# Performance work log

Hardware: AMD Instinct MI355X
Metric: run time of the kernel (lower is better)

Reference implementation:

```python
import jax, jax.numpy as jnp
import numpy as np

EMBED = 128
HEADS = 16
N = 10000
E = 160000
NEG_SLOPE = 0.2


def setup_inputs() -> dict:
    key = jax.random.key(0)
    ks = jax.random.split(key, 12)
    s = 0.05
    return {
        "x": jax.random.normal(ks[0], (N, EMBED), jnp.float32),
        "edge_index": jax.random.randint(ks[1], (2, E), 0, N, jnp.int64),
        # gat1: in=EMBED, out=EMBED, heads=16, concat
        "W1": jax.random.normal(ks[2], (EMBED, HEADS * EMBED), jnp.float32) * s,
        "a_src1": jax.random.normal(ks[3], (HEADS, EMBED), jnp.float32) * s,
        "a_dst1": jax.random.normal(ks[4], (HEADS, EMBED), jnp.float32) * s,
        "b1": jnp.zeros((HEADS * EMBED,), jnp.float32),
        # gat2: in=HEADS*EMBED, out=EMBED, heads=1, no concat
        "W2": jax.random.normal(ks[5], (HEADS * EMBED, EMBED), jnp.float32) * s,
        "a_src2": jax.random.normal(ks[6], (1, EMBED), jnp.float32) * s,
        "a_dst2": jax.random.normal(ks[7], (1, EMBED), jnp.float32) * s,
        "b2": jnp.zeros((EMBED,), jnp.float32),
        # classifier
        "Wc": jax.random.normal(ks[8], (EMBED, 1), jnp.float32) * s,
        "bc": jnp.zeros((1,), jnp.float32),
    }


def _gat_layer(x, src, dst, W, a_src, a_dst, b, heads, out_ch, n_nodes):
    # node projection: [N, H, C]
    h = (x @ W).reshape(n_nodes, heads, out_ch)
    # per-node attention logits [N, H]
    al_s = jnp.einsum('nhc,hc->nh', h, a_src)
    al_d = jnp.einsum('nhc,hc->nh', h, a_dst)
    # per-edge logits [E, H]
    e = jax.nn.leaky_relu(al_s[src] + al_d[dst], NEG_SLOPE)
    # segment softmax over incoming edges of each dst node
    m = jax.ops.segment_max(e, dst, num_segments=n_nodes)
    ex = jnp.exp(e - m[dst])
    z = jax.ops.segment_sum(ex, dst, num_segments=n_nodes)
    alpha = ex / (z[dst] + 1e-16)
    # weighted scatter-aggregate [N, H, C]
    msg = h[src] * alpha[:, :, None]
    out = jax.ops.segment_sum(msg, dst, num_segments=n_nodes)
    return out.reshape(n_nodes, heads * out_ch) + b


def reference(x, edge_index, W1, a_src1, a_dst1, b1, W2, a_src2, a_dst2, b2, Wc, bc):
    n_nodes = x.shape[0]
    # PyG GATConv default: add self loops
    loop = jnp.arange(n_nodes, dtype=edge_index.dtype)
    src = jnp.concatenate([edge_index[0], loop])
    dst = jnp.concatenate([edge_index[1], loop])
    h = _gat_layer(x, src, dst, W1, a_src1, a_dst1, b1, HEADS, EMBED, n_nodes)
    h = jax.nn.elu(h)
    h = _gat_layer(h, src, dst, W2, a_src2, a_dst2, b2, 1, EMBED, n_nodes)
    return h @ Wc + bc  # [N, 1]
```

## Files before the change

kernel.cpp:

```cpp
#include <hip/hip_runtime.h>
#include <hip/hip_bf16.h>

#define EMBED 128
#define HEADS 16
#define NEG 0.2f

typedef __attribute__((ext_vector_type(8))) short short8;
typedef __attribute__((ext_vector_type(4))) float floatx4;
typedef __attribute__((ext_vector_type(2))) float floatx2;

#define GLOAD_LDS16(g, l)                                                                  \
  __builtin_amdgcn_global_load_lds((const __attribute__((address_space(1))) unsigned int*)(g), \
                                   (__attribute__((address_space(3))) unsigned int*)(l),       \
                                   16, 0, 0)

static __device__ __forceinline__ float leaky(float x) { return x > 0.f ? x : NEG * x; }

static __device__ __forceinline__ short f2bf_bits(float f) {
  __hip_bfloat16 h = __float2bfloat16(f);
  union { __hip_bfloat16 b; short s; } u;
  u.b = h;
  return u.s;
}


__global__ __launch_bounds__(256) void k_prep_hist(const float* __restrict__ W1,
                                                   const float* __restrict__ a_src1,
                                                   const float* __restrict__ a_dst1,
                                                   const float* __restrict__ W2,
                                                   const float* __restrict__ a_src2,
                                                   const float* __restrict__ a_dst2,
                                                   const float* __restrict__ Wc,
                                                   const float* __restrict__ b2,
                                                   const float* __restrict__ bc,
                                                   float* __restrict__ wsAll,
                                                   float* __restrict__ uvec,
                                                   float* __restrict__ cconst,
                                                   short* __restrict__ hi,
                                                   short* __restrict__ lo,
                                                   const int* __restrict__ ei, int E, int N,
                                                   int* __restrict__ deg) {
  __shared__ float tile[64][65];
  int bx = blockIdx.x;
  if (bx < 64) {
    int h = bx & 15;
    int c0 = ((bx >> 4) & 1) * 64;
    int j0 = ((bx >> 5) & 1) * 64;
    int t = threadIdx.x;
#pragma unroll
    for (int i = 0; i < 4; ++i) {
      int idx4 = i * 256 + t;
      int c = idx4 >> 4, j4 = idx4 & 15;
      float4 v = *(const float4*)&W1[(size_t)(c0 + c) * 2048 + h * 128 + j0 + j4 * 4];
      tile[c][j4 * 4 + 0] = v.x;
      tile[c][j4 * 4 + 1] = v.y;
      tile[c][j4 * 4 + 2] = v.z;
      tile[c][j4 * 4 + 3] = v.w;
    }
    __syncthreads();
#pragma unroll
    for (int i = 0; i < 4; ++i) {
      int idx = i * 256 + t;
      int j = idx >> 4, c4 = idx & 15;
      unsigned short vh[4], vl[4];
#pragma unroll
      for (int ii = 0; ii < 4; ++ii) {
        float wv = tile[c4 * 4 + ii][j];
        short hb = f2bf_bits(wv);
        float hf = __uint_as_float(((unsigned int)(unsigned short)hb) << 16);
        vh[ii] = (unsigned short)hb;
        vl[ii] = (unsigned short)f2bf_bits(wv - hf);
      }
      size_t o = (size_t)h * 16384 + (size_t)(j0 + j) * 128 + c0 + c4 * 4;
      *(ushort4*)&hi[o] = make_ushort4(vh[0], vh[1], vh[2], vh[3]);
      *(ushort4*)&lo[o] = make_ushort4(vl[0], vl[1], vl[2], vl[3]);
    }
    return;
  }
  if (bx < 105) {
    int gid = (bx - 64) * 256 + threadIdx.x;
    if (gid < 4096) {
      int sel = gid >> 11;
      int id = gid & 2047;
      int h = id >> 7, k = id & 127;
      const float* av = sel ? a_dst1 : a_src1;
      float sum = 0.f;
      const float* wrow = W1 + (size_t)k * 2048 + h * 128;
      const float* arow = av + h * 128;
#pragma unroll 4
      for (int c = 0; c < 128; ++c) sum += wrow[c] * arow[c];
      wsAll[gid] = sum;
    } else if (gid < 10240) {
      int g = gid - 4096;
      int sel = g >> 11;
      int k = g & 2047;
      const float* v = sel == 0 ? Wc : (sel == 1 ? a_src2 : a_dst2);
      const float* wrow = W2 + (size_t)k * 128;
      float s = 0.f;
#pragma unroll 4
      for (int j = 0; j < 128; ++j) s += wrow[j] * v[j];
      uvec[g] = s;
    } else if (gid == 10240) {
      float s = 0.f;
      for (int j = 0; j < 128; ++j) s += b2[j] * Wc[j];
      *cconst = s + bc[0];
    }
    return;
  }
  int i = (bx - 105) * 256 + threadIdx.x;
  int Et = E + N;
  if (i >= Et) return;
  int d = (i < E) ? ei[E + i] : (i - E);
  atomicAdd(&deg[d], 1);
}


__global__ __launch_bounds__(256) void k_scan_al1(const int* __restrict__ deg,
                                                  int* __restrict__ row_ptr,
                                                  int* __restrict__ cursor,
                                                  const float* __restrict__ x,
                                                  const float* __restrict__ wsAll,
                                                  float* __restrict__ als,
                                                  float* __restrict__ ald, int N) {
  __shared__ float wss[128][16], wsd[128][16];
  __shared__ int wsum[4];
  int tid = threadIdx.x;
  int bx = blockIdx.x;

  if (bx == 0) {
    int lane = tid & 63, w = tid >> 6;
    int base = 0;
    for (int c0 = 0; c0 < N; c0 += 1024) {
      int i4 = c0 + tid * 4;
      int a0 = 0, a1 = 0, a2 = 0, a3 = 0;
      if (i4 + 3 < N) {
        int4 v = *(const int4*)&deg[i4];
        a0 = v.x; a1 = v.y; a2 = v.z; a3 = v.w;
      } else {
        if (i4 < N) a0 = deg[i4];
        if (i4 + 1 < N) a1 = deg[i4 + 1];
        if (i4 + 2 < N) a2 = deg[i4 + 2];
        if (i4 + 3 < N) a3 = deg[i4 + 3];
      }
      int tot = a0 + a1 + a2 + a3;
      int s = tot;
#pragma unroll
      for (int dd = 1; dd < 64; dd <<= 1) {
        int t = __shfl_up(s, dd);
        if (lane >= dd) s += t;
      }
      int wexcl = s - tot;
      if (lane == 63) wsum[w] = s;
      __syncthreads();
      int carry = 0, ctot = 0;
#pragma unroll
      for (int k = 0; k < 4; ++k) {
        int t = wsum[k];
        ctot += t;
        if (k < w) carry += t;
      }
      int p0 = base + carry + wexcl;
      int p1 = p0 + a0, p2 = p1 + a1, p3 = p2 + a2;
      if (i4 + 3 < N) {
        *(int4*)&row_ptr[i4] = make_int4(p0, p1, p2, p3);
        *(int4*)&cursor[i4] = make_int4(p0, p1, p2, p3);
      } else {
        if (i4 < N) { row_ptr[i4] = p0; cursor[i4] = p0; }
        if (i4 + 1 < N) { row_ptr[i4 + 1] = p1; cursor[i4 + 1] = p1; }
        if (i4 + 2 < N) { row_ptr[i4 + 2] = p2; cursor[i4 + 2] = p2; }
        if (i4 + 3 < N) { row_ptr[i4 + 3] = p3; cursor[i4 + 3] = p3; }
      }
      base += ctot;
      __syncthreads();
    }
    if (tid == 0) row_ptr[N] = base;
    return;
  }

  for (int i = tid; i < 2048; i += 256) {
    int h = i >> 7, c = i & 127;
    wss[c][h] = wsAll[i];
    wsd[c][h] = wsAll[2048 + i];
  }
  __syncthreads();
  int gid = (bx - 1) * 256 + tid;
  int n = gid >> 4, h = gid & 15;
  if (n >= N) return;
  const float4* xp = (const float4*)(x + (size_t)n * 128);
  float ps = 0.f, pd = 0.f;
#pragma unroll 8
  for (int c4 = 0; c4 < 32; ++c4) {
    float4 xv = xp[c4];
    int c = c4 * 4;
    ps += xv.x * wss[c][h] + xv.y * wss[c + 1][h] + xv.z * wss[c + 2][h] + xv.w * wss[c + 3][h];
    pd += xv.x * wsd[c][h] + xv.y * wsd[c + 1][h] + xv.z * wsd[c + 2][h] + xv.w * wsd[c + 3][h];
  }
  als[gid] = ps;
  ald[gid] = pd;
}


__global__ void k_scatter(const int* __restrict__ ei, int E, int N,
                          int* __restrict__ cursor, int* __restrict__ csr_src) {
  int i = blockIdx.x * blockDim.x + threadIdx.x;
  int Et = E + N;
  if (i >= Et) return;
  int s = (i < E) ? ei[i] : (i - E);
  int d = (i < E) ? ei[E + i] : (i - E);
  int pos = atomicAdd(&cursor[d], 1);
  csr_src[pos] = s;
}


__global__ __launch_bounds__(256) void k_attn1h(const float* __restrict__ x,
                                                const float* __restrict__ als,
                                                const float* __restrict__ ald,
                                                const int* __restrict__ row_ptr,
                                                const int* __restrict__ csr,
                                                __hip_bfloat16* __restrict__ xaggb,
                                                int N) {
  __shared__ float accsh[2][64][37];

  int tid = threadIdx.x;
  int w = tid >> 6, lane = tid & 63;
  int slot = w >> 1, half = w & 1;
  int d = blockIdx.x * 2 + slot;
  bool active = d < N;

  int e0 = 0, deg = 0;
  if (active) {
    e0 = row_ptr[d];
    deg = row_ptr[d + 1] - e0;
  }

  int g = lane >> 4, c8 = lane & 15;
  float4 aldh4 = make_float4(0.f, 0.f, 0.f, 0.f);
  if (active) aldh4 = *(const float4*)&ald[(size_t)d * 16 + g * 4];

  floatx2 acc2[4][4];
  float zacc[4] = {0.f, 0.f, 0.f, 0.f};
#pragma unroll
  for (int hh = 0; hh < 4; ++hh)
#pragma unroll
    for (int i = 0; i < 4; ++i) acc2[hh][i] = (floatx2){0.f, 0.f};

  if (active) {
    int sreg = 0;
    if (lane < deg) sreg = csr[e0 + lane];
    const float* xc = x + c8 * 8;

    int e = half;
    bool have = e < deg;
    float4 alC = make_float4(0.f, 0.f, 0.f, 0.f);
    float4 xaC = alC, xbC = alC;
    if (have) {
      int sC = (e < 64) ? __shfl(sreg, e) : csr[e0 + e];
      alC = *(const float4*)&als[(size_t)sC * 16 + g * 4];
      const float4* xp = (const float4*)(xc + (size_t)sC * 128);
      xaC = xp[0];
      xbC = xp[1];
    }
    while (have) {
      int e2 = e + 2;
      bool have2 = e2 < deg;
      float4 alN = alC, xaN = xaC, xbN = xbC;
      if (have2) {
        int sN = (e2 < 64) ? __shfl(sreg, e2) : csr[e0 + e2];
        alN = *(const float4*)&als[(size_t)sN * 16 + g * 4];
        const float4* xp2 = (const float4*)(xc + (size_t)sN * 128);
        xaN = xp2[0];
        xbN = xp2[1];
      }
      float ev0 = __expf(leaky(alC.x + aldh4.x));
      float ev1 = __expf(leaky(alC.y + aldh4.y));
      float ev2 = __expf(leaky(alC.z + aldh4.z));
      float ev3 = __expf(leaky(alC.w + aldh4.w));
      zacc[0] += ev0; zacc[1] += ev1; zacc[2] += ev2; zacc[3] += ev3;
      floatx2 x0 = {xaC.x, xaC.y}, x1 = {xaC.z, xaC.w};
      floatx2 x2 = {xbC.x, xbC.y}, x3 = {xbC.z, xbC.w};
      floatx2 e20 = {ev0, ev0}, e21 = {ev1, ev1}, e22 = {ev2, ev2}, e23 = {ev3, ev3};
      acc2[0][0] += e20 * x0; acc2[0][1] += e20 * x1; acc2[0][2] += e20 * x2; acc2[0][3] += e20 * x3;
      acc2[1][0] += e21 * x0; acc2[1][1] += e21 * x1; acc2[1][2] += e21 * x2; acc2[1][3] += e21 * x3;
      acc2[2][0] += e22 * x0; acc2[2][1] += e22 * x1; acc2[2][2] += e22 * x2; acc2[2][3] += e22 * x3;
      acc2[3][0] += e23 * x0; acc2[3][1] += e23 * x1; acc2[3][2] += e23 * x2; acc2[3][3] += e23 * x3;
      e = e2;
      have = have2;
      alC = alN;
      xaC = xaN;
      xbC = xbN;
    }
  }

  if (half == 1) {
#pragma unroll
    for (int hh = 0; hh < 4; ++hh) {
#pragma unroll
      for (int i2 = 0; i2 < 4; ++i2) {
        accsh[slot][lane][hh * 8 + i2 * 2] = acc2[hh][i2][0];
        accsh[slot][lane][hh * 8 + i2 * 2 + 1] = acc2[hh][i2][1];
      }
      accsh[slot][lane][32 + hh] = zacc[hh];
    }
  }
  __syncthreads();
  if (half == 0 && active) {
#pragma unroll
    for (int hh = 0; hh < 4; ++hh) {
      int h = g * 4 + hh;
      float z = zacc[hh] + accsh[slot][lane][32 + hh];
      float iz = 1.f / (z + 1e-16f);
      __hip_bfloat16 t[8];
#pragma unroll
      for (int i2 = 0; i2 < 4; ++i2) {
        float v0 = (acc2[hh][i2][0] + accsh[slot][lane][hh * 8 + i2 * 2]) * iz;
        float v1 = (acc2[hh][i2][1] + accsh[slot][lane][hh * 8 + i2 * 2 + 1]) * iz;
        t[i2 * 2] = __float2bfloat16(v0);
        t[i2 * 2 + 1] = __float2bfloat16(v1);
      }
      *(uint4*)(xaggb + (size_t)h * N * 128 + (size_t)d * 128 + c8 * 8) = *(uint4*)t;
    }
  }
}


__global__ __launch_bounds__(256, 2) void k_fused(const __hip_bfloat16* __restrict__ xaggb,
                                                  const short* __restrict__ w1t_hi,
                                                  const short* __restrict__ w1t_lo,
                                                  const float* __restrict__ b1,
                                                  const float* __restrict__ uvec,
                                                  float2* __restrict__ part2,
                                                  float* __restrict__ partd,
                                                  int N) {
  __shared__ float sh[512];
  __shared__ __align__(16) char Bh[32768];
  __shared__ __align__(16) char Bl[32768];
  int tid = threadIdx.x;
  int h = blockIdx.y;
  int n0 = blockIdx.x * 256;

  const char* gbh = (const char*)(w1t_hi + (size_t)h * 16384);
  const char* gbl = (const char*)(w1t_lo + (size_t)h * 16384);
#pragma unroll
  for (int i = 0; i < 8; ++i) {
    int ci = i * 256 + tid;
    int row4 = (ci >> 4) & 15;
    int srcoff = ((ci & ~15) | ((ci & 15) ^ row4)) << 4;
    GLOAD_LDS16(gbh + srcoff, Bh + ci * 16);
    GLOAD_LDS16(gbl + srcoff, Bl + ci * 16);
  }

  for (int i = tid; i < 512; i += 256) {
    int arr = i >> 7, jj = i & 127;
    sh[i] = (arr == 0) ? b1[h * 128 + jj] : uvec[(arr - 1) * 2048 + h * 128 + jj];
  }

  int w = tid >> 6, lane = tid & 63;
  int quad = lane >> 4, l15 = lane & 15;
  int nw = n0 + w * 64;

  const char* abase = (const char*)xaggb + (size_t)h * N * 256;
  short8 a[4][4];
#pragma unroll
  for (int nt = 0; nt < 4; ++nt) {
    int node = nw + nt * 16 + l15;
    if (node >= N) node = N - 1;
    const char* rowp = abase + (size_t)node * 256 + quad * 16;
#pragma unroll
    for (int ks = 0; ks < 4; ++ks)
      a[nt][ks] = *(const short8*)(rowp + ks * 64);
  }
  __syncthreads();

  floatx4 acc[4][8];
#pragma unroll
  for (int jt = 0; jt < 8; ++jt) {
    floatx4 bb = *(const floatx4*)&sh[jt * 16 + quad * 4];
#pragma unroll
    for (int nt = 0; nt < 4; ++nt) acc[nt][jt] = bb;
  }

  __builtin_amdgcn_s_setprio(1);
  for (int ks = 0; ks < 4; ++ks) {
    int xo = (((ks * 4 + quad) ^ l15) << 4);
#pragma unroll
    for (int jt = 0; jt < 8; ++jt) {
      int po = (jt * 16 + l15) * 256 + xo;
      short8 wh = *(const short8*)(Bh + po);
      short8 wl = *(const short8*)(Bl + po);
#pragma unroll
      for (int nt = 0; nt < 4; ++nt) {
        acc[nt][jt] = __builtin_amdgcn_mfma_f32_16x16x32_bf16(wh, a[nt][ks], acc[nt][jt], 0, 0, 0);
        acc[nt][jt] = __builtin_amdgcn_mfma_f32_16x16x32_bf16(wl, a[nt][ks], acc[nt][jt], 0, 0, 0);
      }
    }
  }
  __builtin_amdgcn_s_setprio(0);

  float pc[4] = {0.f, 0.f, 0.f, 0.f};
  float ps[4] = {0.f, 0.f, 0.f, 0.f};
  float pd[4] = {0.f, 0.f, 0.f, 0.f};
#pragma unroll
  for (int jt = 0; jt < 8; ++jt) {
    floatx4 uc = *(const floatx4*)&sh[128 + jt * 16 + quad * 4];
    floatx4 us = *(const floatx4*)&sh[256 + jt * 16 + quad * 4];
    floatx4 ud = *(const floatx4*)&sh[384 + jt * 16 + quad * 4];
#pragma unroll
    for (int nt = 0; nt < 4; ++nt) {
#pragma unroll
      for (int r = 0; r < 4; ++r) {
        float v = acc[nt][jt][r];
        float e = v > 0.f ? v : (__expf(v) - 1.f);
        pc[nt] += e * uc[r];
        ps[nt] += e * us[r];
        pd[nt] += e * ud[r];
      }
    }
  }
#pragma unroll
  for (int nt = 0; nt < 4; ++nt) {
    float c = pc[nt], s = ps[nt], dd = pd[nt];
    c += __shfl_xor(c, 16); c += __shfl_xor(c, 32);
    s += __shfl_xor(s, 16); s += __shfl_xor(s, 32);
    dd += __shfl_xor(dd, 16); dd += __shfl_xor(dd, 32);
    int node = nw + nt * 16 + l15;
    if (quad == 0 && node < N) {
      atomicAdd(&part2[node].x, s);
      atomicAdd(&part2[node].y, c);
      atomicAdd(&partd[node], dd);
    }
  }
}


__global__ __launch_bounds__(256) void k_attn2s(const float2* __restrict__ part2,
                                                const float* __restrict__ partd,
                                                const int* __restrict__ row_ptr,
                                                const int* __restrict__ csr,
                                                const float* __restrict__ cconst,
                                                float* __restrict__ out, int N) {
  int grp = threadIdx.x >> 4, l = threadIdx.x & 15;
  int d = blockIdx.x * 16 + grp;
  if (d >= N) return;
  int e0 = row_ptr[d], deg = row_ptr[d + 1] - e0;
  float aldd = partd[d];
  float z = 0.f, num = 0.f;
  for (int e = l; e < deg; e += 16) {
    int s = csr[e0 + e];
    float2 v2 = part2[s];
    float v = __expf(leaky(v2.x + aldd));
    z += v;
    num += v * v2.y;
  }
#pragma unroll
  for (int off = 8; off; off >>= 1) {
    z += __shfl_xor(z, off);
    num += __shfl_xor(num, off);
  }
  if (l == 0) out[d] = num / (z + 1e-16f) + cconst[0];
}


extern "C" void kernel_launch(void* const* d_in, const int* in_sizes, int n_in,
                              void* d_out, int out_size, void* d_ws, size_t ws_size,
                              hipStream_t stream) {
  const float* x      = (const float*)d_in[0];
  const int*   ei     = (const int*)d_in[1];
  const float* W1     = (const float*)d_in[2];
  const float* a_src1 = (const float*)d_in[3];
  const float* a_dst1 = (const float*)d_in[4];
  const float* b1     = (const float*)d_in[5];
  const float* W2     = (const float*)d_in[6];
  const float* a_src2 = (const float*)d_in[7];
  const float* a_dst2 = (const float*)d_in[8];
  const float* b2     = (const float*)d_in[9];
  const float* Wc     = (const float*)d_in[10];
  const float* bc     = (const float*)d_in[11];

  int N = in_sizes[0] / EMBED;
  int E = in_sizes[1] / 2;
  int Et = E + N;

  char* ws = (char*)d_ws;
  size_t off = 0;
  auto alloc = [&](size_t bytes) -> void* {
    void* p = ws + off;
    off += (bytes + 255) & ~(size_t)255;
    return p;
  };
  __hip_bfloat16* xaggb = (__hip_bfloat16*)alloc((size_t)N * 2048 * 2 + 65536);
  short* w1t_hi = (short*)alloc((size_t)262144 * 2);
  short* w1t_lo = (short*)alloc((size_t)262144 * 2);
  float* wsAll  = (float*)alloc(4096 * 4);
  float* uvec   = (float*)alloc(6144 * 4);
  float* cconst = (float*)alloc(256);
  float* als1   = (float*)alloc((size_t)N * 16 * 4);
  float* ald1   = (float*)alloc((size_t)N * 16 * 4);

  size_t partBytes = (size_t)3 * N * 4;
  size_t degOff = (partBytes + 255) & ~(size_t)255;
  size_t zeroBytes = degOff + (((size_t)N * 4 + 255) & ~(size_t)255);
  char* zreg = (char*)alloc(zeroBytes);
  float* part   = (float*)zreg;
  float2* part2 = (float2*)part;
  float* partd  = part + 2 * N;
  int* deg      = (int*)(zreg + degOff);

  int* row_ptr  = (int*)alloc((size_t)(N + 1) * 4);
  int* cursor   = (int*)alloc((size_t)N * 4);
  int* csr      = (int*)alloc((size_t)Et * 4);

  int nAl1  = (N * 16 + 255) / 256;
  int nHist = (Et + 255) / 256;

  hipMemsetAsync(zreg, 0, zeroBytes, stream);
  k_prep_hist<<<105 + nHist, 256, 0, stream>>>(W1, a_src1, a_dst1, W2, a_src2, a_dst2, Wc,
                                               b2, bc, wsAll, uvec, cconst, w1t_hi, w1t_lo,
                                               ei, E, N, deg);
  k_scan_al1<<<1 + nAl1, 256, 0, stream>>>(deg, row_ptr, cursor, x, wsAll, als1, ald1, N);
  k_scatter<<<(Et + 255) / 256, 256, 0, stream>>>(ei, E, N, cursor, csr);
  k_attn1h<<<(N + 1) / 2, 256, 0, stream>>>(x, als1, ald1, row_ptr, csr, xaggb, N);
  k_fused<<<dim3((N + 255) / 256, 16), 256, 0, stream>>>(xaggb, w1t_hi, w1t_lo, b1, uvec,
                                                         part2, partd, N);
  k_attn2s<<<(N + 15) / 16, 256, 0, stream>>>(part2, partd, row_ptr, csr, cconst,
                                              (float*)d_out, N);
}
```

Baseline: 173.9 us.

## Use one wave per node in attention aggregation and persistent grid for fused GEMM

The first-layer aggregation kernel now gives each destination node a single wave instead of splitting its edges across two waves. This removes the LDS reduction and the block barrier, at the cost of a serial edge loop twice as long per wave. The fused GEMM kernel becomes a persistent grid of 512 blocks, each looping over node chunks for a fixed head. The per-head weights loaded into LDS are then reused across several chunks instead of being reloaded by every block.

```diff
diff --git a/kernel.cpp b/kernel.cpp
--- a/kernel.cpp
+++ b/kernel.cpp
@@ -219,23 +219,16 @@
                                                 const int* __restrict__ csr,
                                                 __hip_bfloat16* __restrict__ xaggb,
                                                 int N) {
-  __shared__ float accsh[2][64][37];
-
   int tid = threadIdx.x;
   int w = tid >> 6, lane = tid & 63;
-  int slot = w >> 1, half = w & 1;
-  int d = blockIdx.x * 2 + slot;
-  bool active = d < N;
-
-  int e0 = 0, deg = 0;
-  if (active) {
-    e0 = row_ptr[d];
-    deg = row_ptr[d + 1] - e0;
-  }
+  int d = blockIdx.x * 4 + w;
+  if (d >= N) return;
+
+  int e0 = row_ptr[d];
+  int deg = row_ptr[d + 1] - e0;
 
   int g = lane >> 4, c8 = lane & 15;
-  float4 aldh4 = make_float4(0.f, 0.f, 0.f, 0.f);
-  if (active) aldh4 = *(const float4*)&ald[(size_t)d * 16 + g * 4];
+  float4 aldh4 = *(const float4*)&ald[(size_t)d * 16 + g * 4];
 
   floatx2 acc2[4][4];
   float zacc[4] = {0.f, 0.f, 0.f, 0.f};
@@ -244,81 +237,63 @@
 #pragma unroll
     for (int i = 0; i < 4; ++i) acc2[hh][i] = (floatx2){0.f, 0.f};
 
-  if (active) {
-    int sreg = 0;
-    if (lane < deg) sreg = csr[e0 + lane];
-    const float* xc = x + c8 * 8;
-
-    int e = half;
-    bool have = e < deg;
-    float4 alC = make_float4(0.f, 0.f, 0.f, 0.f);
-    float4 xaC = alC, xbC = alC;
-    if (have) {
-      int sC = (e < 64) ? __shfl(sreg, e) : csr[e0 + e];
-      alC = *(const float4*)&als[(size_t)sC * 16 + g * 4];
-      const float4* xp = (const float4*)(xc + (size_t)sC * 128);
-      xaC = xp[0];
-      xbC = xp[1];
-    }
-    while (have) {
-      int e2 = e + 2;
-      bool have2 = e2 < deg;
-      float4 alN = alC, xaN = xaC, xbN = xbC;
-      if (have2) {
-        int sN = (e2 < 64) ? __shfl(sreg, e2) : csr[e0 + e2];
-        alN = *(const float4*)&als[(size_t)sN * 16 + g * 4];
-        const float4* xp2 = (const float4*)(xc + (size_t)sN * 128);
-        xaN = xp2[0];
-        xbN = xp2[1];
-      }
-      float ev0 = __expf(leaky(alC.x + aldh4.x));
-      float ev1 = __expf(leaky(alC.y + aldh4.y));
-      float ev2 = __expf(leaky(alC.z + aldh4.z));
-      float ev3 = __expf(leaky(alC.w + aldh4.w));
-      zacc[0] += ev0; zacc[1] += ev1; zacc[2] += ev2; zacc[3] += ev3;
-      floatx2 x0 = {xaC.x, xaC.y}, x1 = {xaC.z, xaC.w};
-      floatx2 x2 = {xbC.x, xbC.y}, x3 = {xbC.z, xbC.w};
-      floatx2 e20 = {ev0, ev0}, e21 = {ev1, ev1}, e22 = {ev2, ev2}, e23 = {ev3, ev3};
-      acc2[0][0] += e20 * x0; acc2[0][1] += e20 * x1; acc2[0][2] += e20 * x2; acc2[0][3] += e20 * x3;
-      acc2[1][0] += e21 * x0; acc2[1][1] += e21 * x1; acc2[1][2] += e21 * x2; acc2[1][3] += e21 * x3;
-      acc2[2][0] += e22 * x0; acc2[2][1] += e22 * x1; acc2[2][2] += e22 * x2; acc2[2][3] += e22 * x3;
-      acc2[3][0] += e23 * x0; acc2[3][1] += e23 * x1; acc2[3][2] += e23 * x2; acc2[3][3] += e23 * x3;
-      e = e2;
-      have = have2;
-      alC = alN;
-      xaC = xaN;
-      xbC = xbN;
-    }
-  }
-
-  if (half == 1) {
-#pragma unroll
-    for (int hh = 0; hh < 4; ++hh) {
-#pragma unroll
-      for (int i2 = 0; i2 < 4; ++i2) {
-        accsh[slot][lane][hh * 8 + i2 * 2] = acc2[hh][i2][0];
-        accsh[slot][lane][hh * 8 + i2 * 2 + 1] = acc2[hh][i2][1];
-      }
-      accsh[slot][lane][32 + hh] = zacc[hh];
-    }
-  }
-  __syncthreads();
-  if (half == 0 && active) {
-#pragma unroll
-    for (int hh = 0; hh < 4; ++hh) {
-      int h = g * 4 + hh;
-      float z = zacc[hh] + accsh[slot][lane][32 + hh];
-      float iz = 1.f / (z + 1e-16f);
-      __hip_bfloat16 t[8];
-#pragma unroll
-      for (int i2 = 0; i2 < 4; ++i2) {
-        float v0 = (acc2[hh][i2][0] + accsh[slot][lane][hh * 8 + i2 * 2]) * iz;
-        float v1 = (acc2[hh][i2][1] + accsh[slot][lane][hh * 8 + i2 * 2 + 1]) * iz;
-        t[i2 * 2] = __float2bfloat16(v0);
-        t[i2 * 2 + 1] = __float2bfloat16(v1);
-      }
-      *(uint4*)(xaggb + (size_t)h * N * 128 + (size_t)d * 128 + c8 * 8) = *(uint4*)t;
-    }
+  int sreg = 0;
+  if (lane < deg) sreg = csr[e0 + lane];
+  const float* xc = x + c8 * 8;
+
+  int e = 0;
+  bool have = e < deg;
+  float4 alC = make_float4(0.f, 0.f, 0.f, 0.f);
+  float4 xaC = alC, xbC = alC;
+  if (have) {
+    int sC = (e < 64) ? __shfl(sreg, e) : csr[e0 + e];
+    alC = *(const float4*)&als[(size_t)sC * 16 + g * 4];
+    const float4* xp = (const float4*)(xc + (size_t)sC * 128);
+    xaC = xp[0];
+    xbC = xp[1];
+  }
+  while (have) {
+    int e2 = e + 1;
+    bool have2 = e2 < deg;
+    float4 alN = alC, xaN = xaC, xbN = xbC;
+    if (have2) {
+      int sN = (e2 < 64) ? __shfl(sreg, e2) : csr[e0 + e2];
+      alN = *(const float4*)&als[(size_t)sN * 16 + g * 4];
+      const float4* xp2 = (const float4*)(xc + (size_t)sN * 128);
+      xaN = xp2[0];
+      xbN = xp2[1];
+    }
+    float ev0 = __expf(leaky(alC.x + aldh4.x));
+    float ev1 = __expf(leaky(alC.y + aldh4.y));
+    float ev2 = __expf(leaky(alC.z + aldh4.z));
+    float ev3 = __expf(leaky(alC.w + aldh4.w));
+    zacc[0] += ev0; zacc[1] += ev1; zacc[2] += ev2; zacc[3] += ev3;
+    floatx2 x0 = {xaC.x, xaC.y}, x1 = {xaC.z, xaC.w};
+    floatx2 x2 = {xbC.x, xbC.y}, x3 = {xbC.z, xbC.w};
+    floatx2 e20 = {ev0, ev0}, e21 = {ev1, ev1}, e22 = {ev2, ev2}, e23 = {ev3, ev3};
+    acc2[0][0] += e20 * x0; acc2[0][1] += e20 * x1; acc2[0][2] += e20 * x2; acc2[0][3] += e20 * x3;
+    acc2[1][0] += e21 * x0; acc2[1][1] += e21 * x1; acc2[1][2] += e21 * x2; acc2[1][3] += e21 * x3;
+    acc2[2][0] += e22 * x0; acc2[2][1] += e22 * x1; acc2[2][2] += e22 * x2; acc2[2][3] += e22 * x3;
+    acc2[3][0] += e23 * x0; acc2[3][1] += e23 * x1; acc2[3][2] += e23 * x2; acc2[3][3] += e23 * x3;
+    e = e2;
+    have = have2;
+    alC = alN;
+    xaC = xaN;
+    xbC = xbN;
+  }
+
+#pragma unroll
+  for (int hh = 0; hh < 4; ++hh) {
+    int h = g * 4 + hh;
+    float z = zacc[hh];
+    float iz = 1.f / (z + 1e-16f);
+    __hip_bfloat16 t[8];
+#pragma unroll
+    for (int i2 = 0; i2 < 4; ++i2) {
+      t[i2 * 2] = __float2bfloat16(acc2[hh][i2][0] * iz);
+      t[i2 * 2 + 1] = __float2bfloat16(acc2[hh][i2][1] * iz);
+    }
+    *(uint4*)(xaggb + (size_t)h * N * 128 + (size_t)d * 128 + c8 * 8) = *(uint4*)t;
   }
 }
 
@@ -335,8 +310,8 @@
   __shared__ __align__(16) char Bh[32768];
   __shared__ __align__(16) char Bl[32768];
   int tid = threadIdx.x;
-  int h = blockIdx.y;
-  int n0 = blockIdx.x * 256;
+  int b = blockIdx.x;
+  int h = b & 15;
 
   const char* gbh = (const char*)(w1t_hi + (size_t)h * 16384);
   const char* gbl = (const char*)(w1t_lo + (size_t)h * 16384);
@@ -348,7 +323,6 @@
     GLOAD_LDS16(gbh + srcoff, Bh + ci * 16);
     GLOAD_LDS16(gbl + srcoff, Bl + ci * 16);
   }
-
   for (int i = tid; i < 512; i += 256) {
     int arr = i >> 7, jj = i & 127;
     sh[i] = (arr == 0) ? b1[h * 128 + jj] : uvec[(arr - 1) * 2048 + h * 128 + jj];
@@ -356,77 +330,86 @@
 
   int w = tid >> 6, lane = tid & 63;
   int quad = lane >> 4, l15 = lane & 15;
-  int nw = n0 + w * 64;
-
   const char* abase = (const char*)xaggb + (size_t)h * N * 256;
-  short8 a[4][4];
-#pragma unroll
-  for (int nt = 0; nt < 4; ++nt) {
-    int node = nw + nt * 16 + l15;
-    if (node >= N) node = N - 1;
-    const char* rowp = abase + (size_t)node * 256 + quad * 16;
-#pragma unroll
-    for (int ks = 0; ks < 4; ++ks)
-      a[nt][ks] = *(const short8*)(rowp + ks * 64);
-  }
-  __syncthreads();
-
-  floatx4 acc[4][8];
-#pragma unroll
-  for (int jt = 0; jt < 8; ++jt) {
-    floatx4 bb = *(const floatx4*)&sh[jt * 16 + quad * 4];
-#pragma unroll
-    for (int nt = 0; nt < 4; ++nt) acc[nt][jt] = bb;
-  }
-
-  __builtin_amdgcn_s_setprio(1);
-  for (int ks = 0; ks < 4; ++ks) {
-    int xo = (((ks * 4 + quad) ^ l15) << 4);
+
+  int nChunks = (N + 255) >> 8;
+  int stride = gridDim.x >> 4;
+  bool first = true;
+  for (int nchunk = b >> 4; nchunk < nChunks; nchunk += stride) {
+    int nw = nchunk * 256 + w * 64;
+
+    short8 a[4][4];
+#pragma unroll
+    for (int nt = 0; nt < 4; ++nt) {
+      int node = nw + nt * 16 + l15;
+      if (node >= N) node = N - 1;
+      const char* rowp = abase + (size_t)node * 256 + quad * 16;
+#pragma unroll
+      for (int ks = 0; ks < 4; ++ks)
+        a[nt][ks] = *(const short8*)(rowp + ks * 64);
+    }
+    if (first) {
+      __syncthreads();
+      first = false;
+    }
+
+    floatx4 acc[4][8];
 #pragma unroll
     for (int jt = 0; jt < 8; ++jt) {
-      int po = (jt * 16 + l15) * 256 + xo;
-      short8 wh = *(const short8*)(Bh + po);
-      short8 wl = *(const short8*)(Bl + po);
+      floatx4 bb = *(const floatx4*)&sh[jt * 16 + quad * 4];
+#pragma unroll
+      for (int nt = 0; nt < 4; ++nt) acc[nt][jt] = bb;
+    }
+
+    __builtin_amdgcn_s_setprio(1);
+    for (int ks = 0; ks < 4; ++ks) {
+      int xo = (((ks * 4 + quad) ^ l15) << 4);
+#pragma unroll
+      for (int jt = 0; jt < 8; ++jt) {
+        int po = (jt * 16 + l15) * 256 + xo;
+        short8 wh = *(const short8*)(Bh + po);
+        short8 wl = *(const short8*)(Bl + po);
+#pragma unroll
+        for (int nt = 0; nt < 4; ++nt) {
+          acc[nt][jt] = __builtin_amdgcn_mfma_f32_16x16x32_bf16(wh, a[nt][ks], acc[nt][jt], 0, 0, 0);
+          acc[nt][jt] = __builtin_amdgcn_mfma_f32_16x16x32_bf16(wl, a[nt][ks], acc[nt][jt], 0, 0, 0);
+        }
+      }
+    }
+    __builtin_amdgcn_s_setprio(0);
+
+    float pc[4] = {0.f, 0.f, 0.f, 0.f};
+    float ps[4] = {0.f, 0.f, 0.f, 0.f};
+    float pd[4] = {0.f, 0.f, 0.f, 0.f};
+#pragma unroll
+    for (int jt = 0; jt < 8; ++jt) {
+      floatx4 uc = *(const floatx4*)&sh[128 + jt * 16 + quad * 4];
+      floatx4 us = *(const floatx4*)&sh[256 + jt * 16 + quad * 4];
+      floatx4 ud = *(const floatx4*)&sh[384 + jt * 16 + quad * 4];
 #pragma unroll
       for (int nt = 0; nt < 4; ++nt) {
-        acc[nt][jt] = __builtin_amdgcn_mfma_f32_16x16x32_bf16(wh, a[nt][ks], acc[nt][jt], 0, 0, 0);
-        acc[nt][jt] = __builtin_amdgcn_mfma_f32_16x16x32_bf16(wl, a[nt][ks], acc[nt][jt], 0, 0, 0);
-      }
-    }
-  }
-  __builtin_amdgcn_s_setprio(0);
-
-  float pc[4] = {0.f, 0.f, 0.f, 0.f};
-  float ps[4] = {0.f, 0.f, 0.f, 0.f};
-  float pd[4] = {0.f, 0.f, 0.f, 0.f};
-#pragma unroll
-  for (int jt = 0; jt < 8; ++jt) {
-    floatx4 uc = *(const floatx4*)&sh[128 + jt * 16 + quad * 4];
-    floatx4 us = *(const floatx4*)&sh[256 + jt * 16 + quad * 4];
-    floatx4 ud = *(const floatx4*)&sh[384 + jt * 16 + quad * 4];
+#pragma unroll
+        for (int r = 0; r < 4; ++r) {
+          float v = acc[nt][jt][r];
+          float e = v > 0.f ? v : (__expf(v) - 1.f);
+          pc[nt] += e * uc[r];
+          ps[nt] += e * us[r];
+          pd[nt] += e * ud[r];
+        }
+      }
+    }
 #pragma unroll
     for (int nt = 0; nt < 4; ++nt) {
-#pragma unroll
-      for (int r = 0; r < 4; ++r) {
-        float v = acc[nt][jt][r];
-        float e = v > 0.f ? v : (__expf(v) - 1.f);
-        pc[nt] += e * uc[r];
-        ps[nt] += e * us[r];
-        pd[nt] += e * ud[r];
-      }
-    }
-  }
-#pragma unroll
-  for (int nt = 0; nt < 4; ++nt) {
-    float c = pc[nt], s = ps[nt], dd = pd[nt];
-    c += __shfl_xor(c, 16); c += __shfl_xor(c, 32);
-    s += __shfl_xor(s, 16); s += __shfl_xor(s, 32);
-    dd += __shfl_xor(dd, 16); dd += __shfl_xor(dd, 32);
-    int node = nw + nt * 16 + l15;
-    if (quad == 0 && node < N) {
-      atomicAdd(&part2[node].x, s);
-      atomicAdd(&part2[node].y, c);
-      atomicAdd(&partd[node], dd);
+      float c = pc[nt], s = ps[nt], dd = pd[nt];
+      c += __shfl_xor(c, 16); c += __shfl_xor(c, 32);
+      s += __shfl_xor(s, 16); s += __shfl_xor(s, 32);
+      dd += __shfl_xor(dd, 16); dd += __shfl_xor(dd, 32);
+      int node = nw + nt * 16 + l15;
+      if (quad == 0 && node < N) {
+        atomicAdd(&part2[node].x, s);
+        atomicAdd(&part2[node].y, c);
+        atomicAdd(&partd[node], dd);
+      }
     }
   }
 }
@@ -518,9 +501,8 @@
                                                ei, E, N, deg);
   k_scan_al1<<<1 + nAl1, 256, 0, stream>>>(deg, row_ptr, cursor, x, wsAll, als1, ald1, N);
   k_scatter<<<(Et + 255) / 256, 256, 0, stream>>>(ei, E, N, cursor, csr);
-  k_attn1h<<<(N + 1) / 2, 256, 0, stream>>>(x, als1, ald1, row_ptr, csr, xaggb, N);
-  k_fused<<<dim3((N + 255) / 256, 16), 256, 0, stream>>>(xaggb, w1t_hi, w1t_lo, b1, uvec,
-                                                         part2, partd, N);
+  k_attn1h<<<(N + 3) / 4, 256, 0, stream>>>(x, als1, ald1, row_ptr, csr, xaggb, N);
+  k_fused<<<512, 256, 0, stream>>>(xaggb, w1t_hi, w1t_lo, b1, uvec, part2, partd, N);
   k_attn2s<<<(N + 15) / 16, 256, 0, stream>>>(part2, partd, row_ptr, csr, cconst,
                                               (float*)d_out, N);
 }
```

After: 180.2 us. +3.6%, slower.
